# Kernel tuning notes

Measured on AMD Instinct MI355X. Metric: run time of the kernel, lower is better.

## Reference

```python
import jax, jax.numpy as jnp
import numpy as np

EPS = 1e-5
TOP_K = 50

def _layernorm(h, g, b):
    mu = jnp.mean(h, axis=-1, keepdims=True)
    var = jnp.mean((h - mu) ** 2, axis=-1, keepdims=True)
    return (h - mu) * jax.lax.rsqrt(var + EPS) * g + b

def setup_inputs() -> dict:
    key = jax.random.key(0)
    ks = jax.random.split(key, 8)
    B, D, E = 16384, 384, 2048
    return {
        "x": jax.random.normal(ks[0], (B, D), jnp.float32),
        "We": jax.random.normal(ks[1], (D, E), jnp.float32) * 0.05,
        "be": jax.random.normal(ks[2], (E,), jnp.float32) * 0.01,
        "g1": jnp.ones((E,), jnp.float32),
        "b1": jnp.zeros((E,), jnp.float32),
        "Wd": jax.random.normal(ks[3], (E, D), jnp.float32) * 0.02,
        "bd": jax.random.normal(ks[4], (D,), jnp.float32) * 0.01,
        "Wb": jax.random.normal(ks[5], (E, D), jnp.float32) * 0.02,
        "bb": jax.random.normal(ks[6], (D,), jnp.float32) * 0.01,
        "g2": jnp.ones((D,), jnp.float32),
        "b2": jnp.zeros((D,), jnp.float32),
    }

def reference(x, We, be, g1, b1, Wd, bd, Wb, bb, g2, b2):
    # encoder: Linear -> LayerNorm -> ReLU
    h = jax.nn.relu(_layernorm(x @ We + be, g1, b1))  # [B, E]
    # top-k sparsification: zero all but top-50 per row (scatter mask, matches torch)
    _, idx = jax.lax.top_k(h, TOP_K)                  # [B, K]
    rows = jnp.arange(h.shape[0])[:, None]
    mask = jnp.zeros_like(h).at[rows, idx].set(1.0)
    sparse = h * mask                                 # [B, E]
    recon = sparse @ Wd + bd                          # [B, D]
    separated = _layernorm(sparse @ Wb + bb, g2, b2)  # [B, D]
    return recon, sparse, separated
```

## Files before the change

### kernel.cpp

```cpp
#include <hip/hip_runtime.h>
#include <hip/hip_bf16.h>
#include <stdint.h>

#define B_D   384
#define B_E   2048
#define TOPK  50
#define LN_EPS 1e-5f
#define NKS   18
#define NKP   12
#define FIX_WINDOW 2e-4f

typedef short bf16x8 __attribute__((ext_vector_type(8)));
typedef float f32x4  __attribute__((ext_vector_type(4)));

__device__ __forceinline__ float wave_sum_f(float v) {
#pragma unroll
    for (int d = 1; d < 64; d <<= 1) v += __shfl_xor(v, d, 64);
    return v;
}
__device__ __forceinline__ int wave_sum_i(int v) {
#pragma unroll
    for (int d = 1; d < 64; d <<= 1) v += __shfl_xor(v, d, 64);
    return v;
}
__device__ __forceinline__ float wave_max_f(float v) {
#pragma unroll
    for (int d = 1; d < 64; d <<= 1) v = fmaxf(v, __shfl_xor(v, d, 64));
    return v;
}

__device__ __forceinline__ ushort f2bf_hi(float v) {
    __hip_bfloat16 b = __float2bfloat16(v);
    return *(ushort*)&b;
}
__device__ __forceinline__ ushort f2bf_lo(float v) {
    __hip_bfloat16 b = __float2bfloat16(v);
    float rem = v - __bfloat162float(b);
    __hip_bfloat16 l = __float2bfloat16(rem);
    return *(ushort*)&l;
}

__device__ __forceinline__ void llds16(const void* g, void* l) {
    __builtin_amdgcn_global_load_lds((const __attribute__((address_space(1))) void*)g,
                                     (__attribute__((address_space(3))) void*)l, 16, 0, 0);
}

__global__ __launch_bounds__(256) void pack_AB(
    const float* __restrict__ x, const float* __restrict__ We,
    ushort* __restrict__ Ap, ushort* __restrict__ Bp, int* __restrict__ cntr)
{
    const int ks = blockIdx.x, yb = blockIdx.y, t = threadIdx.x;
    if (cntr && t == 0 && ks == 0 && yb == 0) *cntr = 0;
    if (yb < 64) {
        const int mt = yb;
#pragma unroll
        for (int q = 0; q < 8; ++q) {
            const int s = q * 256 + t;
            const int m = s & 255, kg = s >> 8;
            const int kp = ks * 64 + kg * 8;
            const int hi = (kp < 384);
            const int ksrc = hi ? kp : kp - 384;
            const float* src = x + (size_t)(mt * 256 + m) * B_D + ksrc;
            float4 v0 = *(const float4*)src;
            float4 v1 = *(const float4*)(src + 4);
            float vv[8] = {v0.x, v0.y, v0.z, v0.w, v1.x, v1.y, v1.z, v1.w};
            ushort o[8];
#pragma unroll
            for (int e = 0; e < 8; ++e)
                o[e] = hi ? f2bf_hi(vv[e]) : f2bf_lo(vv[e]);
            *(uint4*)(Ap + ((size_t)(mt * NKP + ks) * 2048 + s) * 8) = *(uint4*)o;
        }
    } else {
        const int nt = yb - 64;
#pragma unroll
        for (int q = 0; q < 8; ++q) {
            const int s = q * 256 + t;
            const int nl = s & 255, kg = s >> 8;
            const int kp = ks * 64 + kg * 8;
            const int hi = (kp < 384);
            const int ksrc = hi ? kp : kp - 384;
            const int ng = nt * 256 + nl;
            ushort o[8];
#pragma unroll
            for (int e = 0; e < 8; ++e) {
                float v = We[(size_t)(ksrc + e) * B_E + ng];
                o[e] = hi ? f2bf_hi(v) : f2bf_lo(v);
            }
            *(uint4*)(Bp + ((size_t)(nt * NKP + ks) * 2048 + s) * 8) = *(uint4*)o;
        }
    }
}

__global__ __launch_bounds__(512, 2) void enc_mfma256(
    const ushort* __restrict__ Ap, const ushort* __restrict__ Bp,
    const float* __restrict__ be, float* __restrict__ y)
{
    __shared__ __align__(16) ushort As[2][16384];
    __shared__ __align__(16) ushort Bs[2][16384];
    const int t = threadIdx.x, lane = t & 63, w = t >> 6;
    const int wr = w >> 2, wc = w & 3;
    const int gid = blockIdx.x;
    const int swz = (gid & 7) * 64 + (gid >> 3);
    const int nt = swz & 7, mt = swz >> 3;
    const ushort* gA = Ap + (size_t)mt * NKP * 16384;
    const ushort* gB = Bp + (size_t)nt * NKP * 16384;

    f32x4 acc[8][4];
#pragma unroll
    for (int i = 0; i < 8; ++i)
#pragma unroll
        for (int j = 0; j < 4; ++j)
#pragma unroll
            for (int r = 0; r < 4; ++r) acc[i][j][r] = 0.f;

    const int l15 = lane & 15, l4 = lane >> 4;

#define STAGE256(ls_, buf_)                                                     \
    {                                                                           \
        const int lsv = (ls_);                                                  \
        const int ksA = (lsv < 6) ? lsv : lsv - 6;                              \
        const int ksB = (lsv < 12) ? lsv : lsv - 12;                            \
        const ushort* a_src = gA + (size_t)ksA * 16384 + t * 8;                 \
        const ushort* b_src = gB + (size_t)ksB * 16384 + t * 8;                 \
        _Pragma("unroll")                                                       \
        for (int q = 0; q < 4; ++q) {                                           \
            llds16(a_src + q * 4096, &As[buf_][t * 8 + q * 4096]);              \
            llds16(b_src + q * 4096, &Bs[buf_][t * 8 + q * 4096]);              \
        }                                                                       \
    }

    STAGE256(0, 0);
    __syncthreads();

    for (int ls = 0; ls < NKS; ++ls) {
        const int cur = ls & 1;
        if (ls + 1 < NKS) STAGE256(ls + 1, cur ^ 1);
#pragma unroll
        for (int ko = 0; ko < 2; ++ko) {
            const int kg = ko * 4 + l4;
            bf16x8 af[8], bfr[4];
#pragma unroll
            for (int i = 0; i < 8; ++i)
                af[i] = *(const bf16x8*)&As[cur][(kg * 256 + wr * 128 + i * 16 + l15) * 8];
#pragma unroll
            for (int j = 0; j < 4; ++j)
                bfr[j] = *(const bf16x8*)&Bs[cur][(kg * 256 + wc * 64 + j * 16 + l15) * 8];
#pragma unroll
            for (int i = 0; i < 8; ++i)
#pragma unroll
                for (int j = 0; j < 4; ++j)
                    acc[i][j] = __builtin_amdgcn_mfma_f32_16x16x32_bf16(af[i], bfr[j], acc[i][j], 0, 0, 0);
        }
        if (ls + 1 < NKS) __syncthreads();
    }
#undef STAGE256

    float bev[4];
#pragma unroll
    for (int j = 0; j < 4; ++j) bev[j] = be[nt * 256 + wc * 64 + j * 16 + l15];
#pragma unroll
    for (int i = 0; i < 8; ++i)
#pragma unroll
        for (int j = 0; j < 4; ++j)
#pragma unroll
            for (int r = 0; r < 4; ++r) {
                const int row = mt * 256 + wr * 128 + i * 16 + l4 * 4 + r;
                const int col = nt * 256 + wc * 64 + j * 16 + l15;
                y[(size_t)row * B_E + col] = acc[i][j][r] + bev[j];
            }
}

__global__ __launch_bounds__(256) void enc_gemm_f32(
    const float* __restrict__ x, const float* __restrict__ We,
    const float* __restrict__ be, float* __restrict__ y)
{
    __shared__ float As[8][128];
    __shared__ float Bs[8][128];
    const int t  = threadIdx.x;
    const int m0 = blockIdx.y * 128;
    const int n0 = blockIdx.x * 128;
    const int tx = t & 15, ty = t >> 4;
    const int la_m = t >> 1, la_k = (t & 1) * 4;
    const int lb_k = t >> 5, lb_c = (t & 31) * 4;

    float acc[8][8];
#pragma unroll
    for (int i = 0; i < 8; ++i)
#pragma unroll
        for (int j = 0; j < 8; ++j) acc[i][j] = 0.f;

    for (int k0 = 0; k0 < B_D; k0 += 8) {
        float4 a = *(const float4*)&x[(size_t)(m0 + la_m) * B_D + k0 + la_k];
        float4 b = *(const float4*)&We[(size_t)(k0 + lb_k) * B_E + n0 + lb_c];
        __syncthreads();
        As[la_k + 0][la_m] = a.x;
        As[la_k + 1][la_m] = a.y;
        As[la_k + 2][la_m] = a.z;
        As[la_k + 3][la_m] = a.w;
        *(float4*)&Bs[lb_k][lb_c] = b;
        __syncthreads();
#pragma unroll
        for (int kk = 0; kk < 8; ++kk) {
            float4 a0 = *(const float4*)&As[kk][ty * 4];
            float4 a1 = *(const float4*)&As[kk][ty * 4 + 64];
            float4 b0 = *(const float4*)&Bs[kk][tx * 4];
            float4 b1 = *(const float4*)&Bs[kk][tx * 4 + 64];
            float av[8] = {a0.x,a0.y,a0.z,a0.w,a1.x,a1.y,a1.z,a1.w};
            float bv[8] = {b0.x,b0.y,b0.z,b0.w,b1.x,b1.y,b1.z,b1.w};
#pragma unroll
            for (int i = 0; i < 8; ++i)
#pragma unroll
                for (int j = 0; j < 8; ++j)
                    acc[i][j] = fmaf(av[i], bv[j], acc[i][j]);
        }
    }
    float4 beL = *(const float4*)&be[n0 + tx * 4];
    float4 beH = *(const float4*)&be[n0 + 64 + tx * 4];
    float bl[8] = {beL.x,beL.y,beL.z,beL.w,beH.x,beH.y,beH.z,beH.w};
#pragma unroll
    for (int i = 0; i < 8; ++i) {
        int row = m0 + ty * 4 + (i & 3) + (i >> 2) * 64;
        float4 o0 = {acc[i][0]+bl[0], acc[i][1]+bl[1], acc[i][2]+bl[2], acc[i][3]+bl[3]};
        float4 o1 = {acc[i][4]+bl[4], acc[i][5]+bl[5], acc[i][6]+bl[6], acc[i][7]+bl[7]};
        *(float4*)&y[(size_t)row * B_E + n0 + tx * 4]      = o0;
        *(float4*)&y[(size_t)row * B_E + n0 + 64 + tx * 4] = o1;
    }
}

__device__ __forceinline__ int ln_topk_row(
    float (&h)[32], int lane, const float* __restrict__ g1, const float* __restrict__ b1,
    float* __restrict__ row, int* __restrict__ IwR, float* __restrict__ VwR,
    float* __restrict__ ldsv, int* __restrict__ ldsi)
{
    float s = 0.f;
#pragma unroll
    for (int j = 0; j < 32; ++j) s += h[j];
    s = wave_sum_f(s);
    const float mu = s * (1.f / B_E);
    float ss = 0.f;
#pragma unroll
    for (int j = 0; j < 32; ++j) { float d = h[j] - mu; ss += d * d; }
    ss = wave_sum_f(ss);
    const float rstd = rsqrtf(ss * (1.f / B_E) + LN_EPS);
#pragma unroll
    for (int q = 0; q < 8; ++q) {
        float4 g  = *(const float4*)&g1[q * 256 + lane * 4];
        float4 bb = *(const float4*)&b1[q * 256 + lane * 4];
        float gg[4]  = {g.x,g.y,g.z,g.w};
        float bbv[4] = {bb.x,bb.y,bb.z,bb.w};
#pragma unroll
        for (int i = 0; i < 4; ++i) {
            int j = q*4+i;
            h[j] = fmaxf(fmaf((h[j] - mu) * rstd, gg[i], bbv[i]), 0.f);
        }
    }
    float mx = h[0];
#pragma unroll
    for (int j = 1; j < 32; ++j) mx = fmaxf(mx, h[j]);
    mx = wave_max_f(mx);

    float vlo = 0.f, vhi = __uint_as_float(__float_as_uint(mx) + 1u);
    int cl = 2048;
    bool window = false;
    for (int it = 0; it < 20; ++it) {
        float mid = 0.5f * (vlo + vhi);
        if (it == 0 && 2.2f > vlo && 2.2f < vhi) mid = 2.2f;
        if (!(mid > vlo && mid < vhi)) break;
        int c = 0;
#pragma unroll
        for (int j = 0; j < 32; ++j)
            c += (int)__popcll(__ballot(h[j] >= mid));
        if (c >= TOPK) { vlo = mid; cl = c; if (c <= 64) { window = true; break; } }
        else vhi = mid;
    }
    unsigned lo = __float_as_uint(vlo);
    if (!window) {
        unsigned hi = __float_as_uint(vhi);
        while (hi - lo > 1u) {
            const unsigned mid = lo + ((hi - lo) >> 1);
            const float mf = __uint_as_float(mid);
            int c = 0;
#pragma unroll
            for (int j = 0; j < 32; ++j)
                c += (int)__popcll(__ballot(h[j] >= mf));
            if (c >= TOPK) { lo = mid; cl = c; if (c <= 64) break; }
            else hi = mid;
        }
    }
    const float T0 = __uint_as_float(lo);

    unsigned selmask = 0u;
    int flag = 0;
    bool fastSel = (cl <= 64 && T0 > 0.f);

    if (fastSel) {
        ldsv[lane] = -1.f;
        ldsi[lane] = 1 << 20;
        asm volatile("s_waitcnt lgkmcnt(0)" ::: "memory");
        int base = 0;
#pragma unroll
        for (int j = 0; j < 32; ++j) {
            const bool p = (h[j] >= T0);
            const unsigned long long m = __ballot(p);
            if (p) {
                const int pos = base + (int)__popcll(m & ((1ull << lane) - 1ull));
                ldsv[pos] = h[j];
                ldsi[pos] = (j >> 2) * 256 + lane * 4 + (j & 3);
            }
            base += (int)__popcll(m);
        }
        asm volatile("s_waitcnt lgkmcnt(0)" ::: "memory");
        float sv = ldsv[lane];
        int   si = ldsi[lane];
#pragma unroll
        for (int k = 2; k <= 64; k <<= 1) {
#pragma unroll
            for (int jj = k >> 1; jj > 0; jj >>= 1) {
                const float ov = __shfl_xor(sv, jj, 64);
                const int   oi = __shfl_xor(si, jj, 64);
                const bool dirUp = ((lane & k) == 0);
                const bool lower = ((lane & jj) == 0);
                const bool mineBefore = (sv > ov) || (sv == ov && si < oi);
                const bool keep = (lower == dirUp) ? mineBefore : !mineBefore;
                if (!keep) { sv = ov; si = oi; }
            }
        }
        const float T    = __shfl(sv, TOPK - 1, 64);
        const int   idxT = __shfl(si, TOPK - 1, 64);
        float v51;
        if (cl > TOPK) {
            v51 = __shfl(sv, TOPK, 64);
        } else {
            float bb = -1.f;
#pragma unroll
            for (int j = 0; j < 32; ++j) bb = (h[j] < T0) ? fmaxf(bb, h[j]) : bb;
            v51 = wave_max_f(bb);
        }
        flag = (T - v51 < FIX_WINDOW) ? 1 : 0;
#pragma unroll
        for (int j = 0; j < 32; ++j) {
            const int e = (j >> 2) * 256 + lane * 4 + (j & 3);
            if (h[j] > T || (h[j] == T && e <= idxT)) selmask |= (1u << j);
        }
        if (lane < TOPK) { IwR[lane] = si; VwR[lane] = sv; }
    } else {
        const float T = T0;
        int cgt = 0, ceq = 0;
        float below = -1.f;
#pragma unroll
        for (int j = 0; j < 32; ++j) {
            cgt += (h[j] > T); ceq += (h[j] == T);
            if (h[j] < T) below = fmaxf(below, h[j]);
        }
        const int cgt_t = wave_sum_i(cgt);
        const int ceq_t = wave_sum_i(ceq);
        below = wave_max_f(below);
        const int need = TOPK - cgt_t;

        if (cgt_t + ceq_t == TOPK) {
#pragma unroll
            for (int j = 0; j < 32; ++j) if (h[j] >= T) selmask |= (1u << j);
        } else {
            int base = 0;
            for (int q = 0; q < 8; ++q) {
                int tc = 0;
#pragma unroll
                for (int i = 0; i < 4; ++i) tc += (h[q*4+i] == T);
                int ip = tc;
#pragma unroll
                for (int d = 1; d < 64; d <<= 1) {
                    int o = __shfl_up(ip, d, 64);
                    if (lane >= d) ip += o;
                }
                int rk  = base + ip - tc;
                int tot = __shfl(ip, 63, 64);
#pragma unroll
                for (int i = 0; i < 4; ++i) {
                    int j = q*4+i;
                    if (h[j] > T) selmask |= (1u << j);
                    else if (h[j] == T) { if (rk < need) selmask |= (1u << j); rk++; }
                }
                base += tot;
            }
        }
        if (T > 0.f) {
            if (cgt_t + ceq_t != TOPK && ceq_t > need) flag = 1;
            else if (T - below < FIX_WINDOW) flag = 1;
        }
        const int myc = __popc(selmask);
        int ip = myc;
#pragma unroll
        for (int d = 1; d < 64; d <<= 1) {
            int o = __shfl_up(ip, d, 64);
            if (lane >= d) ip += o;
        }
        int pos = ip - myc;
        for (int j = 0; j < 32; ++j) {
            if ((selmask >> j) & 1u) {
                int e = (j >> 2) * 256 + lane * 4 + (j & 3);
                IwR[pos] = e;
                VwR[pos] = h[j];
                pos++;
            }
        }
    }

#pragma unroll
    for (int q = 0; q < 8; ++q) {
        float4 o;
        o.x = ((selmask >> (q*4+0)) & 1u) ? h[q*4+0] : 0.f;
        o.y = ((selmask >> (q*4+1)) & 1u) ? h[q*4+1] : 0.f;
        o.z = ((selmask >> (q*4+2)) & 1u) ? h[q*4+2] : 0.f;
        o.w = ((selmask >> (q*4+3)) & 1u) ? h[q*4+3] : 0.f;
        *(float4*)&row[q * 256 + lane * 4] = o;
    }
    return flag;
}

__global__ __launch_bounds__(256) void topk_packW(
    float* __restrict__ y, const float* __restrict__ g1, const float* __restrict__ b1,
    int* __restrict__ Iw, float* __restrict__ Vw,
    int* __restrict__ rowlist, int* __restrict__ cntr,
    const float* __restrict__ Wd, const float* __restrict__ Wb, uint* __restrict__ Wp,
    int nTopk)
{
    __shared__ float ldsv[4][64];
    __shared__ int   ldsi[4][64];
    const int bid = blockIdx.x;
    const int t = threadIdx.x;
    if (bid >= nTopk) {
        const int e = (bid - nTopk) * 2 + (t >> 7);
        const int tt = t & 127;
#pragma unroll
        for (int j = 0; j < 3; ++j) {
            const int c = tt + 128 * j;
            const ushort d = f2bf_hi(Wd[(size_t)e * B_D + c]);
            const ushort b = f2bf_hi(Wb[(size_t)e * B_D + c]);
            Wp[(size_t)e * B_D + c] = ((uint)b << 16) | (uint)d;
        }
        return;
    }
    const int lane = t & 63;
    const int w = t >> 6;
    const int r = bid * 4 + w;
    float* row = y + (size_t)r * B_E;
    float h[32];
#pragma unroll
    for (int q = 0; q < 8; ++q) {
        float4 v = *(const float4*)&row[q * 256 + lane * 4];
        h[q*4+0] = v.x; h[q*4+1] = v.y; h[q*4+2] = v.z; h[q*4+3] = v.w;
    }
    int flag = ln_topk_row(h, lane, g1, b1, row, Iw + r * TOPK, Vw + r * TOPK,
                           ldsv[w], ldsi[w]);
    if (rowlist && lane == 0 && flag) {
        int p = atomicAdd(cntr, 1);
        rowlist[p] = r;
    }
}

__global__ __launch_bounds__(256) void fixup_recompute(
    const float* __restrict__ x, const float* __restrict__ We, const float* __restrict__ be,
    float* __restrict__ y, const int* __restrict__ rowlist, const int* __restrict__ cntr)
{
    const int nflag = *cntr;
    const int rb = blockIdx.y * 8;
    if (rb >= nflag) return;
    const int nact = min(nflag - rb, 8);
    const int t = threadIdx.x;

    __shared__ float xs[8][B_D];
    __shared__ int   rIdx[8];
    if (t < 8) rIdx[t] = (t < nact) ? rowlist[rb + t] : -1;
    __syncthreads();
#pragma unroll
    for (int i = 0; i < 8; ++i) {
        if (i < nact) {
            const float* src = x + (size_t)rIdx[i] * B_D;
            for (int j = t; j < B_D; j += 256) xs[i][j] = src[j];
        } else {
            for (int j = t; j < B_D; j += 256) xs[i][j] = 0.f;
        }
    }
    __syncthreads();

    const int c = blockIdx.x * 256 + t;
    const float bc = be[c];
    float acc[8];
#pragma unroll
    for (int i = 0; i < 8; ++i) acc[i] = bc;
#pragma unroll 4
    for (int k = 0; k < B_D; ++k) {
        const float w = We[(size_t)k * B_E + c];
#pragma unroll
        for (int i = 0; i < 8; ++i) acc[i] = fmaf(xs[i][k], w, acc[i]);
    }
#pragma unroll
    for (int i = 0; i < 8; ++i)
        if (i < nact) y[(size_t)rIdx[i] * B_E + c] = acc[i];
}

__global__ __launch_bounds__(256) void fixup_select(
    float* __restrict__ y, const float* __restrict__ g1, const float* __restrict__ b1,
    int* __restrict__ Iw, float* __restrict__ Vw,
    const int* __restrict__ rowlist, const int* __restrict__ cntr)
{
    __shared__ float ldsv[4][64];
    __shared__ int   ldsi[4][64];
    const int nflag = *cntr;
    const int w = threadIdx.x >> 6;
    const int lane = threadIdx.x & 63;
    for (int i = blockIdx.x * 4 + w; i < nflag; i += gridDim.x * 4) {
        const int r = rowlist[i];
        float* row = y + (size_t)r * B_E;
        float h[32];
#pragma unroll
        for (int q = 0; q < 8; ++q) {
            float4 v = *(const float4*)&row[q * 256 + lane * 4];
            h[q*4+0] = v.x; h[q*4+1] = v.y; h[q*4+2] = v.z; h[q*4+3] = v.w;
        }
        ln_topk_row(h, lane, g1, b1, row, Iw + r * TOPK, Vw + r * TOPK,
                    ldsv[w], ldsi[w]);
    }
}

__global__ __launch_bounds__(128) void decode_packed(
    const int* __restrict__ Iw, const float* __restrict__ Vw,
    const uint* __restrict__ Wp, const float* __restrict__ bd,
    const float* __restrict__ bbias, const float* __restrict__ g2,
    const float* __restrict__ b2, float* __restrict__ recon, float* __restrict__ sep)
{
    __shared__ int   sI[TOPK];
    __shared__ float sV[TOPK];
    __shared__ float red[2];
    const int r = blockIdx.x, t = threadIdx.x;
    if (t < TOPK) { sI[t] = Iw[r * TOPK + t]; sV[t] = Vw[r * TOPK + t]; }
    __syncthreads();
    float ad[3], ab[3];
#pragma unroll
    for (int j = 0; j < 3; ++j) { ad[j] = bd[t + 128*j]; ab[j] = bbias[t + 128*j]; }
#pragma unroll 2
    for (int i = 0; i < TOPK; ++i) {
        const int   idx = sI[i];
        const float v   = sV[i];
        const uint* wp  = Wp + (size_t)idx * B_D;
#pragma unroll
        for (int j = 0; j < 3; ++j) {
            const uint u = wp[t + 128*j];
            const float wd = __uint_as_float(u << 16);
            const float wb = __uint_as_float(u & 0xFFFF0000u);
            ad[j] = fmaf(v, wd, ad[j]);
            ab[j] = fmaf(v, wb, ab[j]);
        }
    }
#pragma unroll
    for (int j = 0; j < 3; ++j) recon[(size_t)r * B_D + t + 128*j] = ad[j];
    float s = ab[0] + ab[1] + ab[2];
    s = wave_sum_f(s);
    if ((t & 63) == 0) red[t >> 6] = s;
    __syncthreads();
    const float mu = (red[0] + red[1]) * (1.f / B_D);
    __syncthreads();
    float ss = 0.f;
#pragma unroll
    for (int j = 0; j < 3; ++j) { float d = ab[j] - mu; ss += d * d; }
    ss = wave_sum_f(ss);
    if ((t & 63) == 0) red[t >> 6] = ss;
    __syncthreads();
    const float rstd = rsqrtf((red[0] + red[1]) * (1.f / B_D) + LN_EPS);
#pragma unroll
    for (int j = 0; j < 3; ++j) {
        int c = t + 128*j;
        sep[(size_t)r * B_D + c] = fmaf((ab[j] - mu) * rstd, g2[c], b2[c]);
    }
}

__global__ __launch_bounds__(128) void decode_f32(
    const int* __restrict__ Iw, const float* __restrict__ Vw,
    const float* __restrict__ Wd, const float* __restrict__ bd,
    const float* __restrict__ Wb, const float* __restrict__ bbias,
    const float* __restrict__ g2, const float* __restrict__ b2,
    float* __restrict__ recon, float* __restrict__ sep)
{
    __shared__ int   sI[TOPK];
    __shared__ float sV[TOPK];
    __shared__ float red[2];
    const int r = blockIdx.x, t = threadIdx.x;
    if (t < TOPK) { sI[t] = Iw[r * TOPK + t]; sV[t] = Vw[r * TOPK + t]; }
    __syncthreads();
    float ad[3], ab[3];
#pragma unroll
    for (int j = 0; j < 3; ++j) { ad[j] = bd[t + 128*j]; ab[j] = bbias[t + 128*j]; }
#pragma unroll 2
    for (int i = 0; i < TOPK; ++i) {
        const int   idx = sI[i];
        const float v   = sV[i];
        const float* wd = Wd + (size_t)idx * B_D;
        const float* wb = Wb + (size_t)idx * B_D;
#pragma unroll
        for (int j = 0; j < 3; ++j) {
            ad[j] = fmaf(v, wd[t + 128*j], ad[j]);
            ab[j] = fmaf(v, wb[t + 128*j], ab[j]);
        }
    }
#pragma unroll
    for (int j = 0; j < 3; ++j) recon[(size_t)r * B_D + t + 128*j] = ad[j];
    float s = ab[0] + ab[1] + ab[2];
    s = wave_sum_f(s);
    if ((t & 63) == 0) red[t >> 6] = s;
    __syncthreads();
    const float mu = (red[0] + red[1]) * (1.f / B_D);
    __syncthreads();
    float ss = 0.f;
#pragma unroll
    for (int j = 0; j < 3; ++j) { float d = ab[j] - mu; ss += d * d; }
    ss = wave_sum_f(ss);
    if ((t & 63) == 0) red[t >> 6] = ss;
    __syncthreads();
    const float rstd = rsqrtf((red[0] + red[1]) * (1.f / B_D) + LN_EPS);
#pragma unroll
    for (int j = 0; j < 3; ++j) {
        int c = t + 128*j;
        sep[(size_t)r * B_D + c] = fmaf((ab[j] - mu) * rstd, g2[c], b2[c]);
    }
}

__global__ __launch_bounds__(256) void topk_only(
    float* __restrict__ y, const float* __restrict__ g1, const float* __restrict__ b1,
    int* __restrict__ Iw, float* __restrict__ Vw)
{
    __shared__ float ldsv[4][64];
    __shared__ int   ldsi[4][64];
    const int lane = threadIdx.x & 63;
    const int w = threadIdx.x >> 6;
    const int r = blockIdx.x * 4 + w;
    float* row = y + (size_t)r * B_E;
    float h[32];
#pragma unroll
    for (int q = 0; q < 8; ++q) {
        float4 v = *(const float4*)&row[q * 256 + lane * 4];
        h[q*4+0] = v.x; h[q*4+1] = v.y; h[q*4+2] = v.z; h[q*4+3] = v.w;
    }
    ln_topk_row(h, lane, g1, b1, row, Iw + r * TOPK, Vw + r * TOPK, ldsv[w], ldsi[w]);
}

extern "C" void kernel_launch(void* const* d_in, const int* in_sizes, int n_in,
                              void* d_out, int out_size, void* d_ws, size_t ws_size,
                              hipStream_t stream)
{
    const float* x  = (const float*)d_in[0];
    const float* We = (const float*)d_in[1];
    const float* be = (const float*)d_in[2];
    const float* g1 = (const float*)d_in[3];
    const float* b1 = (const float*)d_in[4];
    const float* Wd = (const float*)d_in[5];
    const float* bd = (const float*)d_in[6];
    const float* Wb = (const float*)d_in[7];
    const float* bb = (const float*)d_in[8];
    const float* g2 = (const float*)d_in[9];
    const float* b2 = (const float*)d_in[10];

    const int Brows = in_sizes[0] / B_D;
    float* recon  = (float*)d_out;
    float* sparse = recon + (size_t)Brows * B_D;
    float* sep    = sparse + (size_t)Brows * B_E;

    char* ws = (char*)d_ws;
    int*   Iw      = (int*)ws;
    float* Vw      = (float*)(ws + 3276800);
    int*   rowlist = (int*)(ws + 6619136);
    int*   cntr    = (int*)(ws + 6684672);
    const size_t apOff = 6688768;
    const size_t bpOff = apOff + (size_t)64 * NKP * 2048 * 16;
    const size_t need  = bpOff + (size_t)8 * NKP * 2048 * 16;

    if (ws_size >= need) {
        ushort* Ap = (ushort*)(ws + apOff);
        ushort* Bp = (ushort*)(ws + bpOff);
        uint*   Wp = (uint*)(ws + apOff);
        pack_AB<<<dim3(NKP, 72), dim3(256), 0, stream>>>(x, We, Ap, Bp, cntr);
        enc_mfma256<<<dim3(512), dim3(512), 0, stream>>>(Ap, Bp, be, sparse);
        topk_packW<<<dim3(Brows / 4 + 1024), dim3(256), 0, stream>>>(
            sparse, g1, b1, Iw, Vw, rowlist, cntr, Wd, Wb, Wp, Brows / 4);
        fixup_recompute<<<dim3(8, Brows / 8), dim3(256), 0, stream>>>(x, We, be, sparse, rowlist, cntr);
        fixup_select<<<dim3(256), dim3(256), 0, stream>>>(sparse, g1, b1, Iw, Vw, rowlist, cntr);
        decode_packed<<<dim3(Brows), dim3(128), 0, stream>>>(Iw, Vw, Wp, bd, bb, g2, b2, recon, sep);
    } else {
        enc_gemm_f32<<<dim3(16, 128), dim3(256), 0, stream>>>(x, We, be, sparse);
        topk_only<<<dim3(Brows / 4), dim3(256), 0, stream>>>(sparse, g1, b1, Iw, Vw);
        decode_f32<<<dim3(Brows), dim3(128), 0, stream>>>(Iw, Vw, Wd, bd, Wb, bb, g2, b2, recon, sep);
    }
}
```

Before: 275.0 us.

## Triple-buffer encoder GEMM with half-K stages, waitcnt-based sync and MFMA priority

Restructures the encoder MFMA GEMM main loop. It now runs 36 half-size K stages through a 3-slot LDS ring and keeps two loads in flight. The full __syncthreads is replaced by an explicit vmcnt wait plus s_barrier. A fragments are loaded in two halves interleaved with MFMA bursts under raised s_setprio, aiming to overlap global-to-LDS loads with compute and reduce barrier stalls. LDS use drops from 128KB to 96KB per block, but the loop now takes twice as many barriers.

After: 290.5 us. +5.6%, slower.

```diff
diff --git a/kernel.cpp b/kernel.cpp
--- a/kernel.cpp
+++ b/kernel.cpp
@@ -8,6 +8,7 @@
 #define LN_EPS 1e-5f
 #define NKS   18
 #define NKP   12
+#define NU    36
 #define FIX_WINDOW 2e-4f
 
 typedef short bf16x8 __attribute__((ext_vector_type(8)));
@@ -91,12 +92,12 @@
     }
 }
 
-__global__ __launch_bounds__(512, 2) void enc_mfma256(
+__global__ __launch_bounds__(512, 2) void enc_mfma256_p(
     const ushort* __restrict__ Ap, const ushort* __restrict__ Bp,
     const float* __restrict__ be, float* __restrict__ y)
 {
-    __shared__ __align__(16) ushort As[2][16384];
-    __shared__ __align__(16) ushort Bs[2][16384];
+    __shared__ __align__(16) ushort As[3][8192];
+    __shared__ __align__(16) ushort Bs[3][8192];
     const int t = threadIdx.x, lane = t & 63, w = t >> 6;
     const int wr = w >> 2, wc = w & 3;
     const int gid = blockIdx.x;
@@ -115,45 +116,57 @@
 
     const int l15 = lane & 15, l4 = lane >> 4;
 
-#define STAGE256(ls_, buf_)                                                     \
+#define ISSUE_U(u_)                                                             \
     {                                                                           \
-        const int lsv = (ls_);                                                  \
+        const int uu = (u_);                                                    \
+        const int lsv = uu >> 1, hh = uu & 1, sl = uu % 3;                      \
         const int ksA = (lsv < 6) ? lsv : lsv - 6;                              \
         const int ksB = (lsv < 12) ? lsv : lsv - 12;                            \
-        const ushort* a_src = gA + (size_t)ksA * 16384 + t * 8;                 \
-        const ushort* b_src = gB + (size_t)ksB * 16384 + t * 8;                 \
-        _Pragma("unroll")                                                       \
-        for (int q = 0; q < 4; ++q) {                                           \
-            llds16(a_src + q * 4096, &As[buf_][t * 8 + q * 4096]);              \
-            llds16(b_src + q * 4096, &Bs[buf_][t * 8 + q * 4096]);              \
-        }                                                                       \
-    }
-
-    STAGE256(0, 0);
-    __syncthreads();
-
-    for (int ls = 0; ls < NKS; ++ls) {
-        const int cur = ls & 1;
-        if (ls + 1 < NKS) STAGE256(ls + 1, cur ^ 1);
-#pragma unroll
-        for (int ko = 0; ko < 2; ++ko) {
-            const int kg = ko * 4 + l4;
-            bf16x8 af[8], bfr[4];
-#pragma unroll
-            for (int i = 0; i < 8; ++i)
-                af[i] = *(const bf16x8*)&As[cur][(kg * 256 + wr * 128 + i * 16 + l15) * 8];
+        const ushort* as_ = gA + (size_t)ksA * 16384 + hh * 8192 + t * 8;       \
+        const ushort* bs_ = gB + (size_t)ksB * 16384 + hh * 8192 + t * 8;       \
+        llds16(as_,        &As[sl][t * 8]);                                     \
+        llds16(as_ + 4096, &As[sl][4096 + t * 8]);                              \
+        llds16(bs_,        &Bs[sl][t * 8]);                                     \
+        llds16(bs_ + 4096, &Bs[sl][4096 + t * 8]);                              \
+    }
+
+    ISSUE_U(0);
+    ISSUE_U(1);
+
+    for (int u = 0; u < NU; ++u) {
+        if (u < NU - 1) asm volatile("s_waitcnt vmcnt(4)" ::: "memory");
+        else            asm volatile("s_waitcnt vmcnt(0)" ::: "memory");
+        __builtin_amdgcn_sched_barrier(0);
+        __builtin_amdgcn_s_barrier();
+        __builtin_amdgcn_sched_barrier(0);
+        if (u + 2 < NU) ISSUE_U(u + 2);
+        const int sl = u % 3;
+        bf16x8 bfr[4], af0[4], af1[4];
+#pragma unroll
+        for (int j = 0; j < 4; ++j)
+            bfr[j] = *(const bf16x8*)&Bs[sl][(l4 * 256 + wc * 64 + j * 16 + l15) * 8];
+#pragma unroll
+        for (int i = 0; i < 4; ++i)
+            af0[i] = *(const bf16x8*)&As[sl][(l4 * 256 + wr * 128 + i * 16 + l15) * 8];
+        __builtin_amdgcn_s_setprio(1);
+#pragma unroll
+        for (int i = 0; i < 4; ++i)
 #pragma unroll
             for (int j = 0; j < 4; ++j)
-                bfr[j] = *(const bf16x8*)&Bs[cur][(kg * 256 + wc * 64 + j * 16 + l15) * 8];
-#pragma unroll
-            for (int i = 0; i < 8; ++i)
-#pragma unroll
-                for (int j = 0; j < 4; ++j)
-                    acc[i][j] = __builtin_amdgcn_mfma_f32_16x16x32_bf16(af[i], bfr[j], acc[i][j], 0, 0, 0);
-        }
-        if (ls + 1 < NKS) __syncthreads();
-    }
-#undef STAGE256
+                acc[i][j] = __builtin_amdgcn_mfma_f32_16x16x32_bf16(af0[i], bfr[j], acc[i][j], 0, 0, 0);
+        __builtin_amdgcn_s_setprio(0);
+#pragma unroll
+        for (int i = 0; i < 4; ++i)
+            af1[i] = *(const bf16x8*)&As[sl][(l4 * 256 + wr * 128 + (4 + i) * 16 + l15) * 8];
+        __builtin_amdgcn_s_setprio(1);
+#pragma unroll
+        for (int i = 0; i < 4; ++i)
+#pragma unroll
+            for (int j = 0; j < 4; ++j)
+                acc[4 + i][j] = __builtin_amdgcn_mfma_f32_16x16x32_bf16(af1[i], bfr[j], acc[4 + i][j], 0, 0, 0);
+        __builtin_amdgcn_s_setprio(0);
+    }
+#undef ISSUE_U
 
     float bev[4];
 #pragma unroll
@@ -678,7 +691,7 @@
         ushort* Bp = (ushort*)(ws + bpOff);
         uint*   Wp = (uint*)(ws + apOff);
         pack_AB<<<dim3(NKP, 72), dim3(256), 0, stream>>>(x, We, Ap, Bp, cntr);
-        enc_mfma256<<<dim3(512), dim3(512), 0, stream>>>(Ap, Bp, be, sparse);
+        enc_mfma256_p<<<dim3(512), dim3(512), 0, stream>>>(Ap, Bp, be, sparse);
         topk_packW<<<dim3(Brows / 4 + 1024), dim3(256), 0, stream>>>(
             sparse, g1, b1, Iw, Vw, rowlist, cntr, Wd, Wb, Wp, Brows / 4);
         fixup_recompute<<<dim3(8, Brows / 8), dim3(256), 0, stream>>>(x, We, be, sparse, rowlist, cntr);
```

## Restructure split-bf16 encoder GEMM loop to reuse hi fragments across hi/lo products

Applied to the files above, without the earlier changes.

The encoder MFMA kernel used to stream 18 concatenated K-stages (hi/lo combinations laid out sequentially). It now stages matching hi and lo halves of A and B together and computes Ah*Bh, Ah*Bl and Al*Bh from one stage. The hi fragments are loaded from LDS once and reused for two products, and there are fewer loop iterations and barriers. LDS footprint per stage stays the same, but register pressure rises because more fragment arrays are live at once.

Measured after the change: 267.3 us. 1.03x faster.

```diff
diff --git a/kernel.cpp b/kernel.cpp
--- a/kernel.cpp
+++ b/kernel.cpp
@@ -6,7 +6,6 @@
 #define B_E   2048
 #define TOPK  50
 #define LN_EPS 1e-5f
-#define NKS   18
 #define NKP   12
 #define FIX_WINDOW 2e-4f
 
@@ -91,12 +90,14 @@
     }
 }
 
-__global__ __launch_bounds__(512, 2) void enc_mfma256(
+__global__ __launch_bounds__(512, 2) void enc_mfma256b(
     const ushort* __restrict__ Ap, const ushort* __restrict__ Bp,
     const float* __restrict__ be, float* __restrict__ y)
 {
-    __shared__ __align__(16) ushort As[2][16384];
-    __shared__ __align__(16) ushort Bs[2][16384];
+    __shared__ __align__(16) ushort Ah[2][8192];
+    __shared__ __align__(16) ushort Al[2][8192];
+    __shared__ __align__(16) ushort Bh[2][8192];
+    __shared__ __align__(16) ushort Bl[2][8192];
     const int t = threadIdx.x, lane = t & 63, w = t >> 6;
     const int wr = w >> 2, wc = w & 3;
     const int gid = blockIdx.x;
@@ -115,45 +116,63 @@
 
     const int l15 = lane & 15, l4 = lane >> 4;
 
-#define STAGE256(ls_, buf_)                                                     \
+#define STAGEH(hk_, b_)                                                         \
     {                                                                           \
-        const int lsv = (ls_);                                                  \
-        const int ksA = (lsv < 6) ? lsv : lsv - 6;                              \
-        const int ksB = (lsv < 12) ? lsv : lsv - 12;                            \
-        const ushort* a_src = gA + (size_t)ksA * 16384 + t * 8;                 \
-        const ushort* b_src = gB + (size_t)ksB * 16384 + t * 8;                 \
-        _Pragma("unroll")                                                       \
-        for (int q = 0; q < 4; ++q) {                                           \
-            llds16(a_src + q * 4096, &As[buf_][t * 8 + q * 4096]);              \
-            llds16(b_src + q * 4096, &Bs[buf_][t * 8 + q * 4096]);              \
-        }                                                                       \
-    }
-
-    STAGE256(0, 0);
-    __syncthreads();
-
-    for (int ls = 0; ls < NKS; ++ls) {
-        const int cur = ls & 1;
-        if (ls + 1 < NKS) STAGE256(ls + 1, cur ^ 1);
-#pragma unroll
-        for (int ko = 0; ko < 2; ++ko) {
-            const int kg = ko * 4 + l4;
-            bf16x8 af[8], bfr[4];
-#pragma unroll
-            for (int i = 0; i < 8; ++i)
-                af[i] = *(const bf16x8*)&As[cur][(kg * 256 + wr * 128 + i * 16 + l15) * 8];
+        const int hh = (hk_);                                                   \
+        const int kt = hh >> 1, hf = hh & 1;                                    \
+        const ushort* ah_ = gA + (size_t)kt * 16384 + hf * 8192 + t * 8;        \
+        const ushort* al_ = gA + (size_t)(kt + 6) * 16384 + hf * 8192 + t * 8;  \
+        const ushort* bh_ = gB + (size_t)kt * 16384 + hf * 8192 + t * 8;        \
+        const ushort* bl_ = gB + (size_t)(kt + 6) * 16384 + hf * 8192 + t * 8;  \
+        llds16(ah_,        &Ah[b_][t * 8]);                                     \
+        llds16(ah_ + 4096, &Ah[b_][4096 + t * 8]);                              \
+        llds16(al_,        &Al[b_][t * 8]);                                     \
+        llds16(al_ + 4096, &Al[b_][4096 + t * 8]);                              \
+        llds16(bh_,        &Bh[b_][t * 8]);                                     \
+        llds16(bh_ + 4096, &Bh[b_][4096 + t * 8]);                              \
+        llds16(bl_,        &Bl[b_][t * 8]);                                     \
+        llds16(bl_ + 4096, &Bl[b_][4096 + t * 8]);                              \
+    }
+
+    STAGEH(0, 0);
+    __syncthreads();
+
+    for (int hk = 0; hk < 12; ++hk) {
+        const int sl = hk & 1;
+        if (hk + 1 < 12) STAGEH(hk + 1, sl ^ 1);
+        bf16x8 bhf[4], ahf[8];
+#pragma unroll
+        for (int j = 0; j < 4; ++j)
+            bhf[j] = *(const bf16x8*)&Bh[sl][(l4 * 256 + wc * 64 + j * 16 + l15) * 8];
+#pragma unroll
+        for (int i = 0; i < 8; ++i)
+            ahf[i] = *(const bf16x8*)&Ah[sl][(l4 * 256 + wr * 128 + i * 16 + l15) * 8];
+#pragma unroll
+        for (int i = 0; i < 8; ++i)
 #pragma unroll
             for (int j = 0; j < 4; ++j)
-                bfr[j] = *(const bf16x8*)&Bs[cur][(kg * 256 + wc * 64 + j * 16 + l15) * 8];
-#pragma unroll
-            for (int i = 0; i < 8; ++i)
-#pragma unroll
-                for (int j = 0; j < 4; ++j)
-                    acc[i][j] = __builtin_amdgcn_mfma_f32_16x16x32_bf16(af[i], bfr[j], acc[i][j], 0, 0, 0);
-        }
-        if (ls + 1 < NKS) __syncthreads();
-    }
-#undef STAGE256
+                acc[i][j] = __builtin_amdgcn_mfma_f32_16x16x32_bf16(ahf[i], bhf[j], acc[i][j], 0, 0, 0);
+        bf16x8 blf[4];
+#pragma unroll
+        for (int j = 0; j < 4; ++j)
+            blf[j] = *(const bf16x8*)&Bl[sl][(l4 * 256 + wc * 64 + j * 16 + l15) * 8];
+#pragma unroll
+        for (int i = 0; i < 8; ++i)
+#pragma unroll
+            for (int j = 0; j < 4; ++j)
+                acc[i][j] = __builtin_amdgcn_mfma_f32_16x16x32_bf16(ahf[i], blf[j], acc[i][j], 0, 0, 0);
+        bf16x8 alf[8];
+#pragma unroll
+        for (int i = 0; i < 8; ++i)
+            alf[i] = *(const bf16x8*)&Al[sl][(l4 * 256 + wr * 128 + i * 16 + l15) * 8];
+#pragma unroll
+        for (int i = 0; i < 8; ++i)
+#pragma unroll
+            for (int j = 0; j < 4; ++j)
+                acc[i][j] = __builtin_amdgcn_mfma_f32_16x16x32_bf16(alf[i], bhf[j], acc[i][j], 0, 0, 0);
+        if (hk + 1 < 12) __syncthreads();
+    }
+#undef STAGEH
 
     float bev[4];
 #pragma unroll
@@ -678,7 +697,7 @@
         ushort* Bp = (ushort*)(ws + bpOff);
         uint*   Wp = (uint*)(ws + apOff);
         pack_AB<<<dim3(NKP, 72), dim3(256), 0, stream>>>(x, We, Ap, Bp, cntr);
-        enc_mfma256<<<dim3(512), dim3(512), 0, stream>>>(Ap, Bp, be, sparse);
+        enc_mfma256b<<<dim3(512), dim3(512), 0, stream>>>(Ap, Bp, be, sparse);
         topk_packW<<<dim3(Brows / 4 + 1024), dim3(256), 0, stream>>>(
             sparse, g1, b1, Iw, Vw, rowlist, cntr, Wd, Wb, Wp, Brows / 4);
         fixup_recompute<<<dim3(8, Brows / 8), dim3(256), 0, stream>>>(x, We, be, sparse, rowlist, cntr);
```
